# Kernel tuning notes

Hardware: AMD Instinct MI355X
Metric: run time of the kernel (lower is better)

The kernel has to match this reference:

```python
import jax, jax.numpy as jnp
import numpy as np

N, E, ND, ED, H1, H2 = 50000, 800000, 128, 16, 256, 32
NEG_SLOPE = 0.2


def setup_inputs() -> dict:
    key = jax.random.key(0)
    ks = jax.random.split(key, 12)
    s = lambda k, shape: jax.random.normal(k, shape, jnp.float32) * 0.05
    return dict(
        x=jax.random.normal(ks[0], (N, ND), jnp.float32),
        edge_index=jax.random.randint(ks[1], (2, E), 0, N),
        edge_attr=jax.random.normal(ks[2], (E, ED), jnp.float32),
        Wl1=s(ks[3], (H1, ND)), bl1=jnp.zeros((H1,), jnp.float32),
        Wr1=s(ks[4], (H1, ND)), br1=jnp.zeros((H1,), jnp.float32),
        We1=s(ks[5], (H1, ED)), att1=s(ks[6], (H1,)), bias1=jnp.zeros((H1,), jnp.float32),
        Wl2=s(ks[7], (H2, H1)), bl2=jnp.zeros((H2,), jnp.float32),
        Wr2=s(ks[8], (H2, H1)), br2=jnp.zeros((H2,), jnp.float32),
        We2=s(ks[9], (H2, ED)), att2=s(ks[10], (H2,)), bias2=jnp.zeros((H2,), jnp.float32),
    )


def _gatv2_layer(x, src, dst, ea, Wl, bl, Wr, br, We, att, bias, n):
    # heads=1, concat=True  (PyG GATv2Conv defaults)
    xl = x @ Wl.T + bl                      # [n, C]  source transform
    xr = x @ Wr.T + br                      # [n, C]  target transform
    # per-edge message: x_j + x_i + lin_edge(edge_attr), then LeakyReLU
    m = jax.nn.leaky_relu(xl[src] + xr[dst] + ea @ We.T, NEG_SLOPE)  # [Etot, C]
    logit = m @ att                         # [Etot]
    # segment softmax over destination nodes (numerically stable)
    lmax = jax.ops.segment_max(logit, dst, num_segments=n)
    lmax = jnp.where(jnp.isfinite(lmax), lmax, 0.0)
    a = jnp.exp(logit - lmax[dst])
    denom = jax.ops.segment_sum(a, dst, num_segments=n)
    a = a / denom[dst]                      # self-loops guarantee denom > 0
    # scatter-add of alpha-weighted source features, plus output bias
    return jax.ops.segment_sum(xl[src] * a[:, None], dst, num_segments=n) + bias


def reference(x, edge_index, edge_attr,
              Wl1, bl1, Wr1, br1, We1, att1, bias1,
              Wl2, bl2, Wr2, br2, We2, att2, bias2):
    n = x.shape[0]
    src, dst = edge_index[0], edge_index[1]
    # add_self_loops=True with fill_value='mean': loop attr = mean incoming edge_attr
    deg = jax.ops.segment_sum(jnp.ones_like(dst, jnp.float32), dst, num_segments=n)
    loop_attr = jax.ops.segment_sum(edge_attr, dst, num_segments=n) / jnp.maximum(deg, 1.0)[:, None]
    loop = jnp.arange(n)
    src_f = jnp.concatenate([src, loop])
    dst_f = jnp.concatenate([dst, loop])
    ea = jnp.concatenate([edge_attr, loop_attr], axis=0)
    h = _gatv2_layer(x, src_f, dst_f, ea, Wl1, bl1, Wr1, br1, We1, att1, bias1, n)
    h = _gatv2_layer(h, src_f, dst_f, ea, Wl2, bl2, Wr2, br2, We2, att2, bias2, n)
    return h.mean(axis=0)  # [out_dim]
```

## Files before the change

### kernel.cpp

```cpp
#include <hip/hip_runtime.h>
#include <math.h>

#define N_NODES 50000
#define N_EDGES 800000
#define ND 128
#define ED 16
#define H1 256
#define H2 32

typedef short bf16x8 __attribute__((ext_vector_type(8)));
typedef float f32x4 __attribute__((ext_vector_type(4)));
typedef _Float16 half2v __attribute__((ext_vector_type(2)));
typedef uint uintx4 __attribute__((ext_vector_type(4)));
typedef uint uintx8 __attribute__((ext_vector_type(8)));

__device__ __forceinline__ float dot2h(uint w_, uint ea_v, float c) {
    asm("v_dot2_f32_f16 %0, %1, %2, %0" : "+v"(c) : "v"(w_), "v"(ea_v));
    return c;
}
__device__ __forceinline__ float dot2hs(uint w_, uint ea_s, float c) {
    asm("v_dot2_f32_f16 %0, %2, %1, %0" : "+v"(c) : "v"(w_), "s"(ea_s));
    return c;
}
__device__ __forceinline__ float fmamix_lo(uint a, float b, float c) {
    float d;
    asm("v_fma_mix_f32 %0, %1, %2, %3 op_sel_hi:[1,0,0]" : "=v"(d) : "v"(a), "v"(b), "v"(c));
    return d;
}
__device__ __forceinline__ float fmamix_hi(uint a, float b, float c) {
    float d;
    asm("v_fma_mix_f32 %0, %1, %2, %3 op_sel:[1,0,0] op_sel_hi:[1,0,0]" : "=v"(d) : "v"(a), "v"(b), "v"(c));
    return d;
}
__device__ __forceinline__ ushort f2bf(float f) {
    uint u = __float_as_uint(f);
    return (ushort)((u + 0x7fff + ((u >> 16) & 1)) >> 16);
}
__device__ __forceinline__ float exp2a(float x) {
    float d;
    asm("v_exp_f32 %0, %1" : "=v"(d) : "v"(x));
    return d;
}

__device__ __forceinline__ void sload8(const int* pc, const char* pe,
                                       uintx4& c0, uintx4& c1,
                                       uintx8& e0, uintx8& e1, uintx8& e2, uintx8& e3,
                                       uintx8& e4, uintx8& e5, uintx8& e6, uintx8& e7) {
    asm volatile("s_load_dwordx4 %0, %10, 0x0\n\t"
                 "s_load_dwordx4 %1, %10, 0x10\n\t"
                 "s_load_dwordx8 %2, %11, 0x0\n\t"
                 "s_load_dwordx8 %3, %11, 0x20\n\t"
                 "s_load_dwordx8 %4, %11, 0x40\n\t"
                 "s_load_dwordx8 %5, %11, 0x60\n\t"
                 "s_load_dwordx8 %6, %11, 0x80\n\t"
                 "s_load_dwordx8 %7, %11, 0xa0\n\t"
                 "s_load_dwordx8 %8, %11, 0xc0\n\t"
                 "s_load_dwordx8 %9, %11, 0xe0\n\t"
                 "s_waitcnt lgkmcnt(0)"
                 : "=s"(c0), "=s"(c1), "=s"(e0), "=s"(e1), "=s"(e2), "=s"(e3),
                   "=s"(e4), "=s"(e5), "=s"(e6), "=s"(e7)
                 : "s"(pc), "s"(pe));
}
__device__ __forceinline__ void sload4(const int* pc, const char* pe,
                                       uintx4& c, uintx8& e0, uintx8& e1,
                                       uintx8& e2, uintx8& e3) {
    asm volatile("s_load_dwordx4 %0, %5, 0x0\n\t"
                 "s_load_dwordx8 %1, %6, 0x0\n\t"
                 "s_load_dwordx8 %2, %6, 0x20\n\t"
                 "s_load_dwordx8 %3, %6, 0x40\n\t"
                 "s_load_dwordx8 %4, %6, 0x60\n\t"
                 "s_waitcnt lgkmcnt(0)"
                 : "=s"(c), "=s"(e0), "=s"(e1), "=s"(e2), "=s"(e3)
                 : "s"(pc), "s"(pe));
}

__device__ __forceinline__ uint2 ldx(const _Float16* xlh, uint s, uint laneoff) {
    return *(const uint2*)((const char*)xlh + ((size_t)s << 9) + laneoff);
}
__device__ __forceinline__ int rfl(int v) { return __builtin_amdgcn_readfirstlane(v); }

__global__ void k_deg(const int* __restrict__ ei, int* __restrict__ counts, int E) {
    int e = blockIdx.x * blockDim.x + threadIdx.x;
    if (e < E) atomicAdd(&counts[ei[E + e]], 1);
}

__global__ void k_scan1(const int* __restrict__ counts, int* __restrict__ partial, int n, int chunk) {
    __shared__ int sh[256];
    int beg = blockIdx.x * chunk, end = min(beg + chunk, n);
    int sum = 0;
    for (int i = beg + threadIdx.x; i < end; i += 256) sum += counts[i] + 1;
    sh[threadIdx.x] = sum;
    __syncthreads();
    for (int off = 128; off; off >>= 1) {
        if (threadIdx.x < off) sh[threadIdx.x] += sh[threadIdx.x + off];
        __syncthreads();
    }
    if (threadIdx.x == 0) partial[blockIdx.x] = sh[0];
}
__global__ void k_scan2(int* __restrict__ partial) {
    __shared__ int sh[256];
    int v = partial[threadIdx.x];
    sh[threadIdx.x] = v;
    __syncthreads();
    for (int off = 1; off < 256; off <<= 1) {
        int t = (threadIdx.x >= off) ? sh[threadIdx.x - off] : 0;
        __syncthreads();
        sh[threadIdx.x] += t;
        __syncthreads();
    }
    partial[threadIdx.x] = sh[threadIdx.x] - v;
}
__global__ void k_scan3(const int* __restrict__ counts, const int* __restrict__ partial,
                        int* __restrict__ rowptr, int n, int chunk) {
    __shared__ int sh[256];
    int beg = blockIdx.x * chunk, end = min(beg + chunk, n);
    int run = partial[blockIdx.x];
    for (int base = beg; base < end; base += 256) {
        int i = base + threadIdx.x;
        int v = (i < end) ? counts[i] + 1 : 0;
        sh[threadIdx.x] = v;
        __syncthreads();
        for (int off = 1; off < 256; off <<= 1) {
            int t = (threadIdx.x >= off) ? sh[threadIdx.x - off] : 0;
            __syncthreads();
            sh[threadIdx.x] += t;
            __syncthreads();
        }
        if (i < end) rowptr[i + 1] = run + sh[threadIdx.x];
        __syncthreads();
        run += sh[255];
        __syncthreads();
    }
    if (blockIdx.x == 0 && threadIdx.x == 0) rowptr[0] = 0;
}

__global__ void k_fill_csr(const int* __restrict__ ei, const float* __restrict__ ea,
                           const int* __restrict__ rowptr, int* __restrict__ fill,
                           int* __restrict__ csr_src, _Float16* __restrict__ ea_h, int E, int n) {
    int idx = blockIdx.x * blockDim.x + threadIdx.x;
    if (idx < E) {
        int dst = ei[E + idx];
        int slot = rowptr[dst] + atomicAdd(&fill[dst], 1);
        csr_src[slot] = ei[idx];
        const float* srow = ea + (size_t)idx * ED;
        _Float16* drow = ea_h + (size_t)slot * ED;
        #pragma unroll
        for (int q = 0; q < 4; ++q) {
            float4 f = ((const float4*)srow)[q];
            drow[q * 4 + 0] = (_Float16)f.x;
            drow[q * 4 + 1] = (_Float16)f.y;
            drow[q * 4 + 2] = (_Float16)f.z;
            drow[q * 4 + 3] = (_Float16)f.w;
        }
    } else if (idx < E + n) {
        int i = idx - E;
        csr_src[rowptr[i + 1] - 1] = i;
    }
}

__global__ __launch_bounds__(256) void k_loop_mean(_Float16* __restrict__ ea_h,
                                                   const int* __restrict__ rowptr, int n) {
    int lane = threadIdx.x & 63;
    int wave = (blockIdx.x * blockDim.x + threadIdx.x) >> 6;
    int nwaves = (gridDim.x * blockDim.x) >> 6;
    int g = lane >> 3, q = lane & 7;
    for (int node = wave; node < n; node += nwaves) {
        int beg = rowptr[node], last = rowptr[node + 1] - 1;
        float sx = 0.f, sy = 0.f;
        for (int r = beg + g; r < last; r += 8) {
            uint v = *(const uint*)((const char*)ea_h + ((uint)r << 5) + (q << 2));
            half2v h = __builtin_bit_cast(half2v, v);
            sx += (float)h.x;
            sy += (float)h.y;
        }
        #pragma unroll
        for (int off = 8; off <= 32; off <<= 1) {
            sx += __shfl_xor(sx, off);
            sy += __shfl_xor(sy, off);
        }
        if (lane < 8) {
            int cnt = last - beg;
            float inv = 1.f / (float)(cnt > 0 ? cnt : 1);
            half2v o;
            o.x = (_Float16)(sx * inv);
            o.y = (_Float16)(sy * inv);
            *(uint*)((char*)ea_h + ((uint)last << 5) + (q << 2)) = __builtin_bit_cast(uint, o);
        }
    }
}

__global__ __launch_bounds__(256) void k_pack_all(const float* __restrict__ x,
                                                  const float* __restrict__ Wl1,
                                                  const float* __restrict__ Wr1,
                                                  const float* __restrict__ We1,
                                                  const float* __restrict__ Wl2,
                                                  const float* __restrict__ Wr2,
                                                  const float* __restrict__ We2,
                                                  ushort* __restrict__ x_bf,
                                                  ushort* __restrict__ wcat1,
                                                  ushort* __restrict__ wcat2,
                                                  _Float16* __restrict__ We1_h,
                                                  _Float16* __restrict__ We2_h) {
    const int T4 = N_NODES * ND / 4;
    int idx = blockIdx.x * blockDim.x + threadIdx.x;
    if (idx < T4) {
        float4 f = ((const float4*)x)[idx];
        ushort4 o;
        o.x = f2bf(f.x); o.y = f2bf(f.y); o.z = f2bf(f.z); o.w = f2bf(f.w);
        ((ushort4*)x_bf)[idx] = o;
        return;
    }
    int k = idx - T4;
    if (k < 2 * H1 * ND) {
        int row = k / ND, kk = k - row * ND;
        float v = (row < H1) ? Wl1[(size_t)row * ND + kk] : Wr1[(size_t)(row - H1) * ND + kk];
        wcat1[k] = f2bf(v);
        return;
    }
    k -= 2 * H1 * ND;
    if (k < 2 * H2 * H1) {
        int row = k / H1, kk = k - row * H1;
        float v = (row < H2) ? Wl2[(size_t)row * H1 + kk] : Wr2[(size_t)(row - H2) * H1 + kk];
        wcat2[k] = f2bf(v);
        return;
    }
    k -= 2 * H2 * H1;
    if (k < H1 * ED) { We1_h[k] = (_Float16)We1[k]; return; }
    k -= H1 * ED;
    if (k < H2 * ED) We2_h[k] = (_Float16)We2[k];
}

template <int HALF_A, int HALF_B>
__global__ __launch_bounds__(256) void k_gemm_mfma(const ushort* __restrict__ Xb,
                                                   const ushort* __restrict__ Wc,
                                                   const float* __restrict__ ba,
                                                   const float* __restrict__ bb,
                                                   void* __restrict__ Ya,
                                                   void* __restrict__ Yb,
                                                   int n, int K, int C) {
    int tid = threadIdx.x;
    int lane = tid & 63, wv = tid >> 6;
    int r = lane & 15, kg = lane >> 4;
    int row0 = blockIdx.x * 64 + wv * 16;
    int colblk = blockIdx.y * 64;
    int arow = row0 + r;
    if (arow >= n) arow = n - 1;
    const ushort* aptr = Xb + (size_t)arow * K + kg * 8;
    f32x4 acc[4] = {};
    for (int k0 = 0; k0 < K; k0 += 32) {
        bf16x8 av = *(const bf16x8*)(aptr + k0);
        #pragma unroll
        for (int t = 0; t < 4; ++t) {
            const ushort* bptr = Wc + (size_t)(colblk + t * 16 + r) * K + k0 + kg * 8;
            bf16x8 bv = *(const bf16x8*)bptr;
            acc[t] = __builtin_amdgcn_mfma_f32_16x16x32_bf16(av, bv, acc[t], 0, 0, 0);
        }
    }
    #pragma unroll
    for (int t = 0; t < 4; ++t) {
        int col = colblk + t * 16 + r;
        int rowb = row0 + kg * 4;
        #pragma unroll
        for (int q = 0; q < 4; ++q) {
            int row = rowb + q;
            if (row >= n) continue;
            float v = acc[t][q];
            if (col < C) {
                v += ba[col];
                if (HALF_A) ((_Float16*)Ya)[(size_t)row * C + col] = (_Float16)v;
                else        ((float*)Ya)[(size_t)row * C + col] = v;
            } else {
                v += bb[col - C];
                if (HALF_B) ((_Float16*)Yb)[(size_t)row * C + (col - C)] = (_Float16)v;
                else        ((float*)Yb)[(size_t)row * C + (col - C)] = v;
            }
        }
    }
}

__device__ __forceinline__ float logit_s(const uint (&w)[4][8], uintx8 es,
                                         uint2 xv, float4 xrv, float4 a06, float4 a04) {
    float we0 = 0.f, we1 = 0.f, we2 = 0.f, we3 = 0.f;
    #pragma unroll
    for (int q = 0; q < 8; ++q) {
        we0 = dot2hs(w[0][q], es[q], we0);
        we1 = dot2hs(w[1][q], es[q], we1);
        we2 = dot2hs(w[2][q], es[q], we2);
        we3 = dot2hs(w[3][q], es[q], we3);
    }
    float z0 = fmamix_lo(xv.x, 1.0f, we0 + xrv.x);
    float z1 = fmamix_hi(xv.x, 1.0f, we1 + xrv.y);
    float z2 = fmamix_lo(xv.y, 1.0f, we2 + xrv.z);
    float z3 = fmamix_hi(xv.y, 1.0f, we3 + xrv.w);
    return fmaf(a06.x, z0, fmaf(a04.x, fabsf(z0),
           fmaf(a06.y, z1, fmaf(a04.y, fabsf(z1),
           fmaf(a06.z, z2, fmaf(a04.z, fabsf(z2),
           fmaf(a06.w, z3, a04.w * fabsf(z3))))))));
}
__device__ __forceinline__ float logit_v(const uint (&w)[4][8], uint4 e0, uint4 e1,
                                         uint2 xv, float4 xrv, float4 a06, float4 a04) {
    uint ev[8] = {e0.x, e0.y, e0.z, e0.w, e1.x, e1.y, e1.z, e1.w};
    float we0 = 0.f, we1 = 0.f, we2 = 0.f, we3 = 0.f;
    #pragma unroll
    for (int q = 0; q < 8; ++q) {
        we0 = dot2h(w[0][q], ev[q], we0);
        we1 = dot2h(w[1][q], ev[q], we1);
        we2 = dot2h(w[2][q], ev[q], we2);
        we3 = dot2h(w[3][q], ev[q], we3);
    }
    float z0 = fmamix_lo(xv.x, 1.0f, we0 + xrv.x);
    float z1 = fmamix_hi(xv.x, 1.0f, we1 + xrv.y);
    float z2 = fmamix_lo(xv.y, 1.0f, we2 + xrv.z);
    float z3 = fmamix_hi(xv.y, 1.0f, we3 + xrv.w);
    return fmaf(a06.x, z0, fmaf(a04.x, fabsf(z0),
           fmaf(a06.y, z1, fmaf(a04.y, fabsf(z1),
           fmaf(a06.z, z2, fmaf(a04.z, fabsf(z2),
           fmaf(a06.w, z3, a04.w * fabsf(z3))))))));
}

#define ACC1(X, Q)                                              \
    ac0 = fmamix_lo((X).x, (Q), ac0);                           \
    ac1 = fmamix_hi((X).x, (Q), ac1);                           \
    ac2 = fmamix_lo((X).y, (Q), ac2);                           \
    ac3 = fmamix_hi((X).y, (Q), ac3);

__global__ __launch_bounds__(256) void k_gat1(const _Float16* __restrict__ xlh,
                                              const _Float16* __restrict__ xrh,
                                              const _Float16* __restrict__ ea_h,
                                              const _Float16* __restrict__ We_h,
                                              const float* __restrict__ att,
                                              const float* __restrict__ bias,
                                              const int* __restrict__ rowptr,
                                              const int* __restrict__ csr_src,
                                              ushort* __restrict__ out_bf, int n) {
    const int lane = threadIdx.x & 63;
    int wave = rfl((int)((blockIdx.x * blockDim.x + threadIdx.x) >> 6));
    int nwaves = (gridDim.x * blockDim.x) >> 6;
    const uint* Wp = (const uint*)We_h;
    uint w[4][8];
    #pragma unroll
    for (int r = 0; r < 4; ++r)
        #pragma unroll
        for (int q = 0; q < 8; ++q) w[r][q] = Wp[(lane * 4 + r) * 8 + q];
    const float L2E = 1.44269504088896f;
    float4 attv = ((const float4*)att)[lane];
    float4 bv = ((const float4*)bias)[lane];
    float4 a06, a04;
    a06.x = 0.6f * L2E * attv.x; a06.y = 0.6f * L2E * attv.y;
    a06.z = 0.6f * L2E * attv.z; a06.w = 0.6f * L2E * attv.w;
    a04.x = 0.4f * L2E * attv.x; a04.y = 0.4f * L2E * attv.y;
    a04.z = 0.4f * L2E * attv.z; a04.w = 0.4f * L2E * attv.w;
    const uint laneoff = (uint)lane << 3;
    const char* eab = (const char*)ea_h;

    for (int node = wave; node < n; node += nwaves) {
        uint2 xru = *(const uint2*)((const char*)xrh + ((size_t)node << 9) + laneoff);
        half2v xr0 = __builtin_bit_cast(half2v, xru.x);
        half2v xr1 = __builtin_bit_cast(half2v, xru.y);
        float4 xrv;
        xrv.x = (float)xr0.x; xrv.y = (float)xr0.y;
        xrv.z = (float)xr1.x; xrv.w = (float)xr1.y;
        int beg = rfl(rowptr[node]), end = rfl(rowptr[node + 1]);
        float denom = 0.f, ac0 = 0.f, ac1 = 0.f, ac2 = 0.f, ac3 = 0.f;
        int j = beg;
        for (; j + 7 < end; j += 8) {
            uintx4 c0, c1;
            uintx8 e0, e1, e2, e3, e4, e5, e6, e7;
            sload8(csr_src + j, eab + ((size_t)j << 5), c0, c1, e0, e1, e2, e3, e4, e5, e6, e7);
            uint2 x0 = ldx(xlh, c0[0], laneoff);
            uint2 x1 = ldx(xlh, c0[1], laneoff);
            uint2 x2 = ldx(xlh, c0[2], laneoff);
            uint2 x3 = ldx(xlh, c0[3], laneoff);
            uint2 x4 = ldx(xlh, c1[0], laneoff);
            uint2 x5 = ldx(xlh, c1[1], laneoff);
            uint2 x6 = ldx(xlh, c1[2], laneoff);
            uint2 x7 = ldx(xlh, c1[3], laneoff);
            float p0 = logit_s(w, e0, x0, xrv, a06, a04);
            float p1 = logit_s(w, e1, x1, xrv, a06, a04);
            float p2 = logit_s(w, e2, x2, xrv, a06, a04);
            float p3 = logit_s(w, e3, x3, xrv, a06, a04);
            float p4 = logit_s(w, e4, x4, xrv, a06, a04);
            float p5 = logit_s(w, e5, x5, xrv, a06, a04);
            float p6 = logit_s(w, e6, x6, xrv, a06, a04);
            float p7 = logit_s(w, e7, x7, xrv, a06, a04);
            #pragma unroll
            for (int off = 32; off >= 1; off >>= 1) {
                p0 += __shfl_xor(p0, off); p1 += __shfl_xor(p1, off);
                p2 += __shfl_xor(p2, off); p3 += __shfl_xor(p3, off);
                p4 += __shfl_xor(p4, off); p5 += __shfl_xor(p5, off);
                p6 += __shfl_xor(p6, off); p7 += __shfl_xor(p7, off);
            }
            float q0 = exp2a(p0), q1 = exp2a(p1), q2 = exp2a(p2), q3 = exp2a(p3);
            float q4 = exp2a(p4), q5 = exp2a(p5), q6 = exp2a(p6), q7 = exp2a(p7);
            denom += ((q0 + q1) + (q2 + q3)) + ((q4 + q5) + (q6 + q7));
            ACC1(x0, q0) ACC1(x1, q1) ACC1(x2, q2) ACC1(x3, q3)
            ACC1(x4, q4) ACC1(x5, q5) ACC1(x6, q6) ACC1(x7, q7)
        }
        if (j + 3 < end) {
            uintx4 c0;
            uintx8 e0, e1, e2, e3;
            sload4(csr_src + j, eab + ((size_t)j << 5), c0, e0, e1, e2, e3);
            uint2 x0 = ldx(xlh, c0[0], laneoff);
            uint2 x1 = ldx(xlh, c0[1], laneoff);
            uint2 x2 = ldx(xlh, c0[2], laneoff);
            uint2 x3 = ldx(xlh, c0[3], laneoff);
            float p0 = logit_s(w, e0, x0, xrv, a06, a04);
            float p1 = logit_s(w, e1, x1, xrv, a06, a04);
            float p2 = logit_s(w, e2, x2, xrv, a06, a04);
            float p3 = logit_s(w, e3, x3, xrv, a06, a04);
            #pragma unroll
            for (int off = 32; off >= 1; off >>= 1) {
                p0 += __shfl_xor(p0, off); p1 += __shfl_xor(p1, off);
                p2 += __shfl_xor(p2, off); p3 += __shfl_xor(p3, off);
            }
            float q0 = exp2a(p0), q1 = exp2a(p1), q2 = exp2a(p2), q3 = exp2a(p3);
            denom += (q0 + q1) + (q2 + q3);
            ACC1(x0, q0) ACC1(x1, q1) ACC1(x2, q2) ACC1(x3, q3)
            j += 4;
        }
        for (; j < end; ++j) {
            int s0 = rfl(csr_src[j]);
            const uint4* eP = (const uint4*)(eab + ((size_t)(uint)j << 5));
            uint4 e00 = eP[0], e01 = eP[1];
            uint2 x0 = ldx(xlh, (uint)s0, laneoff);
            float p0 = logit_v(w, e00, e01, x0, xrv, a06, a04);
            #pragma unroll
            for (int off = 32; off >= 1; off >>= 1) p0 += __shfl_xor(p0, off);
            float q0 = exp2a(p0);
            denom += q0;
            ACC1(x0, q0)
        }
        float inv = 1.f / denom;
        ushort4 o;
        o.x = f2bf(fmaf(ac0, inv, bv.x));
        o.y = f2bf(fmaf(ac1, inv, bv.y));
        o.z = f2bf(fmaf(ac2, inv, bv.z));
        o.w = f2bf(fmaf(ac3, inv, bv.w));
        *(ushort4*)(out_bf + ((size_t)node << 8) + (lane << 2)) = o;
    }
}

__global__ __launch_bounds__(256) void k_gat2(const float* __restrict__ xl,
                                              const float* __restrict__ xr,
                                              const _Float16* __restrict__ ea_h,
                                              const _Float16* __restrict__ We_h,
                                              const float* __restrict__ att,
                                              const float* __restrict__ bias,
                                              const int* __restrict__ rowptr,
                                              const int* __restrict__ csr_src,
                                              float* __restrict__ out, int n) {
    int tid = threadIdx.x;
    int lane = tid & 63;
    int sub = lane >> 5, c = lane & 31;
    int wave = (blockIdx.x * blockDim.x + tid) >> 6;
    int nwaves = (gridDim.x * blockDim.x) >> 6;
    const uint* Wp = (const uint*)We_h;
    uint w0 = Wp[c * 8 + 0], w1 = Wp[c * 8 + 1], w2 = Wp[c * 8 + 2], w3 = Wp[c * 8 + 3];
    uint w4 = Wp[c * 8 + 4], w5 = Wp[c * 8 + 5], w6 = Wp[c * 8 + 6], w7 = Wp[c * 8 + 7];
    const float L2E = 1.44269504088896f;
    float attc = att[c];
    float a06 = 0.6f * L2E * attc, a04 = 0.4f * L2E * attc;
    float bc = bias[c];

    for (int node = wave; node < n; node += nwaves) {
        float xrc = xr[((size_t)node << 5) + c];
        int beg = rowptr[node], end = rowptr[node + 1];
        float denom = 0.f, acc = 0.f;
        int j = beg;
        for (; j + 3 < end; j += 4) {
            int jA = j + sub, jB = j + 2 + sub;
            int sA = csr_src[jA], sB = csr_src[jB];
            const uint4* ePA = (const uint4*)((const char*)ea_h + ((uint)jA << 5));
            const uint4* ePB = (const uint4*)((const char*)ea_h + ((uint)jB << 5));
            uint4 a0 = ePA[0], a1 = ePA[1];
            uint4 b0 = ePB[0], b1 = ePB[1];
            float xlA = *(const float*)((const char*)xl + (((uint)sA << 7) + (c << 2)));
            float xlB = *(const float*)((const char*)xl + (((uint)sB << 7) + (c << 2)));
            float weA = dot2h(w7, a1.w, dot2h(w6, a1.z, dot2h(w5, a1.y, dot2h(w4, a1.x,
                        dot2h(w3, a0.w, dot2h(w2, a0.z, dot2h(w1, a0.y, dot2h(w0, a0.x, 0.f))))))));
            float weB = dot2h(w7, b1.w, dot2h(w6, b1.z, dot2h(w5, b1.y, dot2h(w4, b1.x,
                        dot2h(w3, b0.w, dot2h(w2, b0.z, dot2h(w1, b0.y, dot2h(w0, b0.x, 0.f))))))));
            float zA = xlA + xrc + weA;
            float zB = xlB + xrc + weB;
            float pA = fmaf(a06, zA, a04 * fabsf(zA));
            float pB = fmaf(a06, zB, a04 * fabsf(zB));
            #pragma unroll
            for (int off = 16; off >= 1; off >>= 1) {
                pA += __shfl_xor(pA, off);
                pB += __shfl_xor(pB, off);
            }
            float qA = exp2a(pA), qB = exp2a(pB);
            denom += qA + qB;
            acc = fmaf(qA, xlA, fmaf(qB, xlB, acc));
        }
        for (; j < end; j += 2) {
            int jj = j + sub;
            bool act = jj < end;
            int js = act ? jj : j;
            int s = csr_src[js];
            const uint4* eP = (const uint4*)((const char*)ea_h + ((uint)js << 5));
            uint4 e0 = eP[0], e1 = eP[1];
            float xlv = *(const float*)((const char*)xl + (((uint)s << 7) + (c << 2)));
            float we = dot2h(w7, e1.w, dot2h(w6, e1.z, dot2h(w5, e1.y, dot2h(w4, e1.x,
                       dot2h(w3, e0.w, dot2h(w2, e0.z, dot2h(w1, e0.y, dot2h(w0, e0.x, 0.f))))))));
            float z = xlv + xrc + we;
            float p = fmaf(a06, z, a04 * fabsf(z));
            #pragma unroll
            for (int off = 16; off >= 1; off >>= 1) p += __shfl_xor(p, off);
            float pe = act ? exp2a(p) : 0.f;
            denom += pe;
            acc = fmaf(pe, xlv, acc);
        }
        acc += __shfl_xor(acc, 32);
        denom += __shfl_xor(denom, 32);
        if (sub == 0) out[((size_t)node << 5) + c] = acc / denom + bc;
    }
}

__global__ __launch_bounds__(256) void k_mean(const float* __restrict__ h2,
                                              float* __restrict__ out, int total, float invN) {
    __shared__ float red[H2];
    int tid = threadIdx.x;
    if (tid < H2) red[tid] = 0.f;
    __syncthreads();
    float part = 0.f;
    for (int idx = blockIdx.x * blockDim.x + tid; idx < total; idx += gridDim.x * blockDim.x)
        part += h2[idx];
    atomicAdd(&red[tid & 31], part);
    __syncthreads();
    if (tid < H2) atomicAdd(&out[tid], red[tid] * invN);
}

extern "C" void kernel_launch(void* const* d_in, const int* in_sizes, int n_in,
                              void* d_out, int out_size, void* d_ws, size_t ws_size,
                              hipStream_t stream) {
    const float* x   = (const float*)d_in[0];
    const int*   ei  = (const int*)d_in[1];
    const float* ea  = (const float*)d_in[2];
    const float* Wl1 = (const float*)d_in[3];
    const float* bl1 = (const float*)d_in[4];
    const float* Wr1 = (const float*)d_in[5];
    const float* br1 = (const float*)d_in[6];
    const float* We1 = (const float*)d_in[7];
    const float* at1 = (const float*)d_in[8];
    const float* bi1 = (const float*)d_in[9];
    const float* Wl2 = (const float*)d_in[10];
    const float* bl2 = (const float*)d_in[11];
    const float* Wr2 = (const float*)d_in[12];
    const float* br2 = (const float*)d_in[13];
    const float* We2 = (const float*)d_in[14];
    const float* at2 = (const float*)d_in[15];
    const float* bi2 = (const float*)d_in[16];
    float* out = (float*)d_out;

    const int N = N_NODES, E = N_EDGES, ET = N_EDGES + N_NODES;
    const int SCAN_CHUNK = (N + 255) / 256;

    size_t off = 0;
    auto carve = [&](size_t bytes) {
        void* p = (char*)d_ws + off;
        off += (bytes + 255) & ~(size_t)255;
        return p;
    };
    int*      counts  = (int*)carve((size_t)N * 4);
    int*      fill    = (int*)carve((size_t)N * 4);
    int*      rowptr  = (int*)carve((size_t)(N + 1) * 4);
    int*      partial = (int*)carve(256 * 4);
    int*      csr_src = (int*)carve((size_t)ET * 4);
    _Float16* ea_h    = (_Float16*)carve((size_t)ET * ED * 2);
    _Float16* We1_h   = (_Float16*)carve((size_t)H1 * ED * 2);
    _Float16* We2_h   = (_Float16*)carve((size_t)H2 * ED * 2);
    ushort*   x_bf    = (ushort*)carve((size_t)N * ND * 2);
    ushort*   wcat1   = (ushort*)carve((size_t)2 * H1 * ND * 2);
    ushort*   wcat2   = (ushort*)carve((size_t)2 * H2 * H1 * 2);
    _Float16* xl1h    = (_Float16*)carve((size_t)N * H1 * 2);
    _Float16* xr1h    = (_Float16*)carve((size_t)N * H1 * 2);
    ushort*   h1_bf   = (ushort*)carve((size_t)N * H1 * 2);
    float*    xl2     = (float*)carve((size_t)N * H2 * 4);
    float*    xr2     = (float*)carve((size_t)N * H2 * 4);
    float*    h2      = (float*)carve((size_t)N * H2 * 4);

    size_t zspan = (size_t)((char*)fill - (char*)counts) + (size_t)N * 4;
    hipMemsetAsync(counts, 0, zspan, stream);
    hipMemsetAsync(out, 0, (size_t)H2 * 4, stream);

    k_deg<<<(E + 255) / 256, 256, 0, stream>>>(ei, counts, E);
    k_scan1<<<256, 256, 0, stream>>>(counts, partial, N, SCAN_CHUNK);
    k_scan2<<<1, 256, 0, stream>>>(partial);
    k_scan3<<<256, 256, 0, stream>>>(counts, partial, rowptr, N, SCAN_CHUNK);
    k_fill_csr<<<(E + N + 255) / 256, 256, 0, stream>>>(ei, ea, rowptr, fill, csr_src, ea_h, E, N);
    k_loop_mean<<<1024, 256, 0, stream>>>(ea_h, rowptr, N);

    const int T4 = N_NODES * ND / 4;
    const int TS = 2 * H1 * ND + 2 * H2 * H1 + H1 * ED + H2 * ED;
    k_pack_all<<<(T4 + TS + 255) / 256, 256, 0, stream>>>(x, Wl1, Wr1, We1, Wl2, Wr2, We2,
                                                          x_bf, wcat1, wcat2, We1_h, We2_h);

    k_gemm_mfma<1, 1><<<dim3((N + 63) / 64, (2 * H1) / 64), 256, 0, stream>>>(
        x_bf, wcat1, bl1, br1, (void*)xl1h, (void*)xr1h, N, ND, H1);
    k_gat1<<<4096, 256, 0, stream>>>(xl1h, xr1h, ea_h, We1_h, at1, bi1,
                                     rowptr, csr_src, h1_bf, N);

    k_gemm_mfma<0, 0><<<dim3((N + 63) / 64, (2 * H2) / 64), 256, 0, stream>>>(
        h1_bf, wcat2, bl2, br2, (void*)xl2, (void*)xr2, N, H1, H2);
    k_gat2<<<12500, 256, 0, stream>>>(xl2, xr2, ea_h, We2_h, at2, bi2,
                                      rowptr, csr_src, h2, N);

    k_mean<<<128, 256, 0, stream>>>(h2, out, N * H2, 1.0f / (float)N);
}
```

Measured before the change: 427.6 us.

## Fuse prep kernels, register-cache GEMM A tile, fold mean into GAT2

Merges degree counting with the x/weight packing into one prep kernel. The GEMM now keeps the A rows in registers and loops over all column blocks inside one block, so the 1D grid no longer reloads A for every column block. GAT2 accumulates per-block channel sums and writes them to a small partial buffer, which a one-block reduction turns into the mean; this drops the h2 round trip and the atomic mean kernel. It also packs fp16 edge-attribute stores into 16-byte writes and switches address math to 32-bit. The cost is fewer GAT2 blocks and a serial final reduction; the 32-bit offsets stay within range for these sizes.

Measured after the change: 472.1 us. +10.4%, slower.

```diff
diff --git a/kernel.cpp b/kernel.cpp
--- a/kernel.cpp
+++ b/kernel.cpp
@@ -7,6 +7,7 @@
 #define ED 16
 #define H1 256
 #define H2 32
+#define GAT2_BLOCKS 2048
 
 typedef short bf16x8 __attribute__((ext_vector_type(8)));
 typedef float f32x4 __attribute__((ext_vector_type(4)));
@@ -75,13 +76,56 @@
 }
 
 __device__ __forceinline__ uint2 ldx(const _Float16* xlh, uint s, uint laneoff) {
-    return *(const uint2*)((const char*)xlh + ((size_t)s << 9) + laneoff);
+    return *(const uint2*)((const char*)xlh + ((s << 9) + laneoff));
 }
 __device__ __forceinline__ int rfl(int v) { return __builtin_amdgcn_readfirstlane(v); }
 
-__global__ void k_deg(const int* __restrict__ ei, int* __restrict__ counts, int E) {
-    int e = blockIdx.x * blockDim.x + threadIdx.x;
-    if (e < E) atomicAdd(&counts[ei[E + e]], 1);
+__global__ __launch_bounds__(256) void k_prep(const int* __restrict__ ei,
+                                              int* __restrict__ counts,
+                                              const float* __restrict__ x,
+                                              const float* __restrict__ Wl1,
+                                              const float* __restrict__ Wr1,
+                                              const float* __restrict__ We1,
+                                              const float* __restrict__ Wl2,
+                                              const float* __restrict__ Wr2,
+                                              const float* __restrict__ We2,
+                                              ushort* __restrict__ x_bf,
+                                              ushort* __restrict__ wcat1,
+                                              ushort* __restrict__ wcat2,
+                                              _Float16* __restrict__ We1_h,
+                                              _Float16* __restrict__ We2_h) {
+    const int T4 = N_NODES * ND / 4;
+    int idx = blockIdx.x * blockDim.x + threadIdx.x;
+    if (idx < N_EDGES) {
+        atomicAdd(&counts[ei[N_EDGES + idx]], 1);
+        return;
+    }
+    int k = idx - N_EDGES;
+    if (k < T4) {
+        float4 f = ((const float4*)x)[k];
+        ushort4 o;
+        o.x = f2bf(f.x); o.y = f2bf(f.y); o.z = f2bf(f.z); o.w = f2bf(f.w);
+        ((ushort4*)x_bf)[k] = o;
+        return;
+    }
+    k -= T4;
+    if (k < 2 * H1 * ND) {
+        int row = k / ND, kk = k - row * ND;
+        float v = (row < H1) ? Wl1[(size_t)row * ND + kk] : Wr1[(size_t)(row - H1) * ND + kk];
+        wcat1[k] = f2bf(v);
+        return;
+    }
+    k -= 2 * H1 * ND;
+    if (k < 2 * H2 * H1) {
+        int row = k / H1, kk = k - row * H1;
+        float v = (row < H2) ? Wl2[(size_t)row * H1 + kk] : Wr2[(size_t)(row - H2) * H1 + kk];
+        wcat2[k] = f2bf(v);
+        return;
+    }
+    k -= 2 * H2 * H1;
+    if (k < H1 * ED) { We1_h[k] = (_Float16)We1[k]; return; }
+    k -= H1 * ED;
+    if (k < H2 * ED) We2_h[k] = (_Float16)We2[k];
 }
 
 __global__ void k_scan1(const int* __restrict__ counts, int* __restrict__ partial, int n, int chunk) {
@@ -143,15 +187,16 @@
         int slot = rowptr[dst] + atomicAdd(&fill[dst], 1);
         csr_src[slot] = ei[idx];
         const float* srow = ea + (size_t)idx * ED;
-        _Float16* drow = ea_h + (size_t)slot * ED;
+        uint o[8];
         #pragma unroll
         for (int q = 0; q < 4; ++q) {
             float4 f = ((const float4*)srow)[q];
-            drow[q * 4 + 0] = (_Float16)f.x;
-            drow[q * 4 + 1] = (_Float16)f.y;
-            drow[q * 4 + 2] = (_Float16)f.z;
-            drow[q * 4 + 3] = (_Float16)f.w;
-        }
+            o[2 * q + 0] = __builtin_bit_cast(uint, __builtin_amdgcn_cvt_pkrtz(f.x, f.y));
+            o[2 * q + 1] = __builtin_bit_cast(uint, __builtin_amdgcn_cvt_pkrtz(f.z, f.w));
+        }
+        uint4* drow = (uint4*)(ea_h + (size_t)slot * ED);
+        drow[0] = make_uint4(o[0], o[1], o[2], o[3]);
+        drow[1] = make_uint4(o[4], o[5], o[6], o[7]);
     } else if (idx < E + n) {
         int i = idx - E;
         csr_src[rowptr[i + 1] - 1] = i;
@@ -189,90 +234,55 @@
     }
 }
 
-__global__ __launch_bounds__(256) void k_pack_all(const float* __restrict__ x,
-                                                  const float* __restrict__ Wl1,
-                                                  const float* __restrict__ Wr1,
-                                                  const float* __restrict__ We1,
-                                                  const float* __restrict__ Wl2,
-                                                  const float* __restrict__ Wr2,
-                                                  const float* __restrict__ We2,
-                                                  ushort* __restrict__ x_bf,
-                                                  ushort* __restrict__ wcat1,
-                                                  ushort* __restrict__ wcat2,
-                                                  _Float16* __restrict__ We1_h,
-                                                  _Float16* __restrict__ We2_h) {
-    const int T4 = N_NODES * ND / 4;
-    int idx = blockIdx.x * blockDim.x + threadIdx.x;
-    if (idx < T4) {
-        float4 f = ((const float4*)x)[idx];
-        ushort4 o;
-        o.x = f2bf(f.x); o.y = f2bf(f.y); o.z = f2bf(f.z); o.w = f2bf(f.w);
-        ((ushort4*)x_bf)[idx] = o;
-        return;
-    }
-    int k = idx - T4;
-    if (k < 2 * H1 * ND) {
-        int row = k / ND, kk = k - row * ND;
-        float v = (row < H1) ? Wl1[(size_t)row * ND + kk] : Wr1[(size_t)(row - H1) * ND + kk];
-        wcat1[k] = f2bf(v);
-        return;
-    }
-    k -= 2 * H1 * ND;
-    if (k < 2 * H2 * H1) {
-        int row = k / H1, kk = k - row * H1;
-        float v = (row < H2) ? Wl2[(size_t)row * H1 + kk] : Wr2[(size_t)(row - H2) * H1 + kk];
-        wcat2[k] = f2bf(v);
-        return;
-    }
-    k -= 2 * H2 * H1;
-    if (k < H1 * ED) { We1_h[k] = (_Float16)We1[k]; return; }
-    k -= H1 * ED;
-    if (k < H2 * ED) We2_h[k] = (_Float16)We2[k];
-}
-
-template <int HALF_A, int HALF_B>
+template <int K, int HALF_A, int HALF_B>
 __global__ __launch_bounds__(256) void k_gemm_mfma(const ushort* __restrict__ Xb,
                                                    const ushort* __restrict__ Wc,
                                                    const float* __restrict__ ba,
                                                    const float* __restrict__ bb,
                                                    void* __restrict__ Ya,
                                                    void* __restrict__ Yb,
-                                                   int n, int K, int C) {
+                                                   int n, int C, int numCB) {
     int tid = threadIdx.x;
     int lane = tid & 63, wv = tid >> 6;
     int r = lane & 15, kg = lane >> 4;
     int row0 = blockIdx.x * 64 + wv * 16;
-    int colblk = blockIdx.y * 64;
     int arow = row0 + r;
     if (arow >= n) arow = n - 1;
     const ushort* aptr = Xb + (size_t)arow * K + kg * 8;
-    f32x4 acc[4] = {};
-    for (int k0 = 0; k0 < K; k0 += 32) {
-        bf16x8 av = *(const bf16x8*)(aptr + k0);
+    bf16x8 av[K / 32];
+    #pragma unroll
+    for (int kb = 0; kb < K / 32; ++kb) av[kb] = *(const bf16x8*)(aptr + kb * 32);
+
+    for (int cb = 0; cb < numCB; ++cb) {
+        int colblk = cb * 64;
+        f32x4 acc[4] = {};
+        #pragma unroll
+        for (int kb = 0; kb < K / 32; ++kb) {
+            #pragma unroll
+            for (int t = 0; t < 4; ++t) {
+                const ushort* bptr = Wc + (size_t)(colblk + t * 16 + r) * K + kb * 32 + kg * 8;
+                bf16x8 bv = *(const bf16x8*)bptr;
+                acc[t] = __builtin_amdgcn_mfma_f32_16x16x32_bf16(av[kb], bv, acc[t], 0, 0, 0);
+            }
+        }
         #pragma unroll
         for (int t = 0; t < 4; ++t) {
-            const ushort* bptr = Wc + (size_t)(colblk + t * 16 + r) * K + k0 + kg * 8;
-            bf16x8 bv = *(const bf16x8*)bptr;
-            acc[t] = __builtin_amdgcn_mfma_f32_16x16x32_bf16(av, bv, acc[t], 0, 0, 0);
-        }
-    }
-    #pragma unroll
-    for (int t = 0; t < 4; ++t) {
-        int col = colblk + t * 16 + r;
-        int rowb = row0 + kg * 4;
-        #pragma unroll
-        for (int q = 0; q < 4; ++q) {
-            int row = rowb + q;
-            if (row >= n) continue;
-            float v = acc[t][q];
-            if (col < C) {
-                v += ba[col];
-                if (HALF_A) ((_Float16*)Ya)[(size_t)row * C + col] = (_Float16)v;
-                else        ((float*)Ya)[(size_t)row * C + col] = v;
-            } else {
-                v += bb[col - C];
-                if (HALF_B) ((_Float16*)Yb)[(size_t)row * C + (col - C)] = (_Float16)v;
-                else        ((float*)Yb)[(size_t)row * C + (col - C)] = v;
+            int col = colblk + t * 16 + r;
+            int rowb = row0 + kg * 4;
+            #pragma unroll
+            for (int q = 0; q < 4; ++q) {
+                int row = rowb + q;
+                if (row >= n) continue;
+                float v = acc[t][q];
+                if (col < C) {
+                    v += ba[col];
+                    if (HALF_A) ((_Float16*)Ya)[(size_t)row * C + col] = (_Float16)v;
+                    else        ((float*)Ya)[(size_t)row * C + col] = v;
+                } else {
+                    v += bb[col - C];
+                    if (HALF_B) ((_Float16*)Yb)[(size_t)row * C + (col - C)] = (_Float16)v;
+                    else        ((float*)Yb)[(size_t)row * C + (col - C)] = v;
+                }
             }
         }
     }
@@ -354,7 +364,7 @@
     const char* eab = (const char*)ea_h;
 
     for (int node = wave; node < n; node += nwaves) {
-        uint2 xru = *(const uint2*)((const char*)xrh + ((size_t)node << 9) + laneoff);
+        uint2 xru = *(const uint2*)((const char*)xrh + (((uint)node << 9) + laneoff));
         half2v xr0 = __builtin_bit_cast(half2v, xru.x);
         half2v xr1 = __builtin_bit_cast(half2v, xru.y);
         float4 xrv;
@@ -436,7 +446,7 @@
         o.y = f2bf(fmaf(ac1, inv, bv.y));
         o.z = f2bf(fmaf(ac2, inv, bv.z));
         o.w = f2bf(fmaf(ac3, inv, bv.w));
-        *(ushort4*)(out_bf + ((size_t)node << 8) + (lane << 2)) = o;
+        *(ushort4*)(out_bf + (((uint)node << 8) + (lane << 2))) = o;
     }
 }
 
@@ -448,7 +458,7 @@
                                               const float* __restrict__ bias,
                                               const int* __restrict__ rowptr,
                                               const int* __restrict__ csr_src,
-                                              float* __restrict__ out, int n) {
+                                              float* __restrict__ partial, int n) {
     int tid = threadIdx.x;
     int lane = tid & 63;
     int sub = lane >> 5, c = lane & 31;
@@ -461,9 +471,10 @@
     float attc = att[c];
     float a06 = 0.6f * L2E * attc, a04 = 0.4f * L2E * attc;
     float bc = bias[c];
+    float msum = 0.f;
 
     for (int node = wave; node < n; node += nwaves) {
-        float xrc = xr[((size_t)node << 5) + c];
+        float xrc = xr[((uint)node << 5) + c];
         int beg = rowptr[node], end = rowptr[node + 1];
         float denom = 0.f, acc = 0.f;
         int j = beg;
@@ -513,22 +524,31 @@
         }
         acc += __shfl_xor(acc, 32);
         denom += __shfl_xor(denom, 32);
-        if (sub == 0) out[((size_t)node << 5) + c] = acc / denom + bc;
-    }
-}
-
-__global__ __launch_bounds__(256) void k_mean(const float* __restrict__ h2,
-                                              float* __restrict__ out, int total, float invN) {
-    __shared__ float red[H2];
-    int tid = threadIdx.x;
-    if (tid < H2) red[tid] = 0.f;
+        msum += acc / denom + bc;
+    }
+    __shared__ float sh[H2];
+    if (tid < H2) sh[tid] = 0.f;
     __syncthreads();
-    float part = 0.f;
-    for (int idx = blockIdx.x * blockDim.x + tid; idx < total; idx += gridDim.x * blockDim.x)
-        part += h2[idx];
-    atomicAdd(&red[tid & 31], part);
+    if (sub == 0) atomicAdd(&sh[c], msum);
     __syncthreads();
-    if (tid < H2) atomicAdd(&out[tid], red[tid] * invN);
+    if (tid < H2) partial[blockIdx.x * H2 + tid] = sh[tid];
+}
+
+__global__ __launch_bounds__(256) void k_mean2(const float* __restrict__ partial,
+                                               float* __restrict__ out) {
+    __shared__ float sh[8][H2];
+    int t = threadIdx.x;
+    int ch = t & 31, seg = t >> 5;
+    float s = 0.f;
+    for (int i = seg; i < GAT2_BLOCKS; i += 8) s += partial[i * H2 + ch];
+    sh[seg][ch] = s;
+    __syncthreads();
+    if (t < H2) {
+        float tot = 0.f;
+        #pragma unroll
+        for (int g = 0; g < 8; ++g) tot += sh[g][ch];
+        out[ch] = tot * (1.f / (float)N_NODES);
+    }
 }
 
 extern "C" void kernel_launch(void* const* d_in, const int* in_sizes, int n_in,
@@ -578,33 +598,30 @@
     ushort*   h1_bf   = (ushort*)carve((size_t)N * H1 * 2);
     float*    xl2     = (float*)carve((size_t)N * H2 * 4);
     float*    xr2     = (float*)carve((size_t)N * H2 * 4);
-    float*    h2      = (float*)carve((size_t)N * H2 * 4);
+    float*    mpart   = (float*)carve((size_t)GAT2_BLOCKS * H2 * 4);
 
     size_t zspan = (size_t)((char*)fill - (char*)counts) + (size_t)N * 4;
     hipMemsetAsync(counts, 0, zspan, stream);
-    hipMemsetAsync(out, 0, (size_t)H2 * 4, stream);
-
-    k_deg<<<(E + 255) / 256, 256, 0, stream>>>(ei, counts, E);
+
+    const int T4 = N_NODES * ND / 4;
+    const int TS = 2 * H1 * ND + 2 * H2 * H1 + H1 * ED + H2 * ED;
+    k_prep<<<(E + T4 + TS + 255) / 256, 256, 0, stream>>>(ei, counts, x, Wl1, Wr1, We1,
+                                                          Wl2, Wr2, We2, x_bf, wcat1, wcat2,
+                                                          We1_h, We2_h);
     k_scan1<<<256, 256, 0, stream>>>(counts, partial, N, SCAN_CHUNK);
     k_scan2<<<1, 256, 0, stream>>>(partial);
     k_scan3<<<256, 256, 0, stream>>>(counts, partial, rowptr, N, SCAN_CHUNK);
     k_fill_csr<<<(E + N + 255) / 256, 256, 0, stream>>>(ei, ea, rowptr, fill, csr_src, ea_h, E, N);
     k_loop_mean<<<1024, 256, 0, stream>>>(ea_h, rowptr, N);
 
-    const int T4 = N_NODES * ND / 4;
-    const int TS = 2 * H1 * ND + 2 * H2 * H1 + H1 * ED + H2 * ED;
-    k_pack_all<<<(T4 + TS + 255) / 256, 256, 0, stream>>>(x, Wl1, Wr1, We1, Wl2, Wr2, We2,
-                                                          x_bf, wcat1, wcat2, We1_h, We2_h);
-
-    k_gemm_mfma<1, 1><<<dim3((N + 63) / 64, (2 * H1) / 64), 256, 0, stream>>>(
-        x_bf, wcat1, bl1, br1, (void*)xl1h, (void*)xr1h, N, ND, H1);
+    k_gemm_mfma<ND, 1, 1><<<(N + 63) / 64, 256, 0, stream>>>(
+        x_bf, wcat1, bl1, br1, (void*)xl1h, (void*)xr1h, N, H1, (2 * H1) / 64);
     k_gat1<<<4096, 256, 0, stream>>>(xl1h, xr1h, ea_h, We1_h, at1, bi1,
                                      rowptr, csr_src, h1_bf, N);
 
-    k_gemm_mfma<0, 0><<<dim3((N + 63) / 64, (2 * H2) / 64), 256, 0, stream>>>(
-        h1_bf, wcat2, bl2, br2, (void*)xl2, (void*)xr2, N, H1, H2);
-    k_gat2<<<12500, 256, 0, stream>>>(xl2, xr2, ea_h, We2_h, at2, bi2,
-                                      rowptr, csr_src, h2, N);
-
-    k_mean<<<128, 256, 0, stream>>>(h2, out, N * H2, 1.0f / (float)N);
-}
+    k_gemm_mfma<H1, 0, 0><<<(N + 63) / 64, 256, 0, stream>>>(
+        h1_bf, wcat2, bl2, br2, (void*)xl2, (void*)xr2, N, H2, (2 * H2) / 64);
+    k_gat2<<<GAT2_BLOCKS, 256, 0, stream>>>(xl2, xr2, ea_h, We2_h, at2, bi2,
+                                            rowptr, csr_src, mpart, N);
+    k_mean2<<<1, 256, 0, stream>>>(mpart, out);
+}
```
